# Kernel optimization log

Hardware: AMD Instinct MI355X
Metric: run time of the kernel (lower is better)

## Reference

```python
import jax, jax.numpy as jnp
import numpy as np

T, B, E, H = 2048, 2, 1024, 16
D = E // H  # head_dim = 64

def setup_inputs() -> dict:
    key = jax.random.key(0)
    ks = jax.random.split(key, 9)
    s = 1.0 / np.sqrt(E)
    return {
        "query": jax.random.normal(ks[0], (T, B, E), dtype=jnp.float32),
        "Wq": jax.random.normal(ks[1], (E, E), dtype=jnp.float32) * s,
        "bq": jax.random.normal(ks[2], (E,), dtype=jnp.float32) * 0.02,
        "Wk": jax.random.normal(ks[3], (E, E), dtype=jnp.float32) * s,
        "bk": jax.random.normal(ks[4], (E,), dtype=jnp.float32) * 0.02,
        "Wv": jax.random.normal(ks[5], (E, E), dtype=jnp.float32) * s,
        "bv": jax.random.normal(ks[6], (E,), dtype=jnp.float32) * 0.02,
        "Wo": jax.random.normal(ks[7], (E, E), dtype=jnp.float32) * s,
        "bo": jax.random.normal(ks[8], (E,), dtype=jnp.float32) * 0.02,
    }

def reference(query, Wq, bq, Wk, bk, Wv, bv, Wo, bo):
    # query: [T, B, E] (fairseq Time x Batch x Channel layout)
    t, b, e = query.shape
    scaling = D ** -0.5
    q = (query @ Wq.T + bq) * scaling          # [T,B,E], scaled like fairseq
    k = query @ Wk.T + bk                      # self-attention: k,v from query
    v = query @ Wv.T + bv
    # split heads: [T,B,H,D]
    q = q.reshape(t, b, H, D)
    k = k.reshape(t, b, H, D)
    v = v.reshape(t, b, H, D)
    # attn weights: [B,H,T(tgt),S(src)]
    scores = jnp.einsum("tbhd,sbhd->bhts", q, k)
    probs = jax.nn.softmax(scores, axis=-1)
    # attend: [T,B,H,D] -> [T,B,E]
    ctx = jnp.einsum("bhts,sbhd->tbhd", probs, v).reshape(t, b, e)
    return ctx @ Wo.T + bo                     # [T,B,E]
```

## Files before the change

kernel.cpp:

```cpp
#include <hip/hip_runtime.h>
#include <hip/hip_bf16.h>
#include <math.h>

#define TT 2048
#define BB 2
#define EE 1024
#define HH 16
#define DD 64
#define RR (TT*BB)

typedef __bf16 bf16x8 __attribute__((ext_vector_type(8)));
typedef float  floatx4 __attribute__((ext_vector_type(4)));

__device__ __forceinline__ unsigned short f2b(float f) {
    union { float f; unsigned u; } x{f};
    return (unsigned short)((x.u + 0x7FFFu + ((x.u >> 16) & 1u)) >> 16);
}
__device__ __forceinline__ float b2f_lo(unsigned u) {
    union { unsigned u; float f; } x{u << 16}; return x.f;
}
__device__ __forceinline__ float b2f_hi(unsigned u) {
    union { unsigned u; float f; } x{u & 0xffff0000u}; return x.f;
}

__device__ __forceinline__ float exp2_fast(float x) {
    return __builtin_amdgcn_exp2f(x);
}

typedef const __attribute__((address_space(1))) unsigned int as1_u32;
typedef __attribute__((address_space(3))) unsigned int as3_u32;
__device__ __forceinline__ void gload16(const void* g, void* l) {
    __builtin_amdgcn_global_load_lds((as1_u32*)g, (as3_u32*)l, 16, 0, 0);
}

#define SCALE_Q 0.18033688011112042f

__device__ __forceinline__ int swz(int r) {
    return (r & 7) ^ (((r >> 3) & 3) << 1);
}

__global__ __launch_bounds__(256)
void pack_bf16(const float* __restrict__ x,  const float* __restrict__ wq,
               const float* __restrict__ wk, const float* __restrict__ wv,
               const float* __restrict__ wo, unsigned short* __restrict__ base,
               unsigned short* __restrict__ wob)
{
    const size_t M4 = (size_t)4 << 20, M7 = (size_t)7 << 20;
    const size_t e0 = ((size_t)blockIdx.x * 256 + threadIdx.x) * 8;
    const float* src;
    unsigned short* dst;
    if (e0 < M4) {
        src = x + e0; dst = base + e0;
    } else if (e0 < M7) {
        const int seg = (int)((e0 >> 20) - 4);
        const float* wsrc[3] = {wq, wk, wv};
        src = wsrc[seg] + (e0 & ((1u << 20) - 1));
        dst = base + e0;
    } else {
        src = wo + (e0 - M7); dst = wob + (e0 - M7);
    }
    const float4 a = *(const float4*)src;
    const float4 b = *(const float4*)(src + 4);
    union { unsigned short u[8]; uint4 v; } p;
    p.u[0] = f2b(a.x); p.u[1] = f2b(a.y); p.u[2] = f2b(a.z); p.u[3] = f2b(a.w);
    p.u[4] = f2b(b.x); p.u[5] = f2b(b.y); p.u[6] = f2b(b.z); p.u[7] = f2b(b.w);
    *(uint4*)dst = p.v;
}

template<int MODE>
__global__ __launch_bounds__(256)
void gemm_mfma(const unsigned short* __restrict__ A,
               const unsigned short* __restrict__ Bw,
               const float* __restrict__ b0, const float* __restrict__ b1,
               const float* __restrict__ b2,
               void* __restrict__ out0, void* __restrict__ out1,
               void* __restrict__ out2)
{
    constexpr int BM = 128;
    constexpr int BN = (MODE == 0) ? 128 : 64;
    constexpr int MT = 4;
    constexpr int NT = (MODE == 0) ? 4 : 2;
    constexpr int RA = BM / 32;
    constexpr int RB = BN / 32;
    constexpr int SMEM = (MODE == 0) ? 34816 : 24576;
    __shared__ __align__(16) unsigned char smem[SMEM];
    unsigned short* ldsA = (unsigned short*)smem;
    unsigned short* ldsB = (unsigned short*)(smem + BM * 128);

    const int tid  = threadIdx.x;
    const int w    = tid >> 6;
    const int lane = tid & 63;
    const int quad = lane >> 4;
    const int l15  = lane & 15;
    const int wm   = w & 1;
    const int wn   = w >> 1;
    const int i0   = blockIdx.x * BM;
    const int j0   = blockIdx.y * BN;

    const unsigned short* ga[RA];
    const unsigned short* gb[RB];
    #pragma unroll
    for (int r = 0; r < RA; ++r) {
        const int slot = r * 256 + tid;
        const int row  = slot >> 3;
        const int gc   = (slot & 7) ^ swz(row);
        ga[r] = A + (size_t)(i0 + row) * EE + gc * 8;
    }
    #pragma unroll
    for (int r = 0; r < RB; ++r) {
        const int slot = r * 256 + tid;
        const int row  = slot >> 3;
        const int gc   = (slot & 7) ^ swz(row);
        gb[r] = Bw + (size_t)(j0 + row) * EE + gc * 8;
    }

    int ofsA[2][MT], ofsB[2][NT];
    #pragma unroll
    for (int mt = 0; mt < MT; ++mt) {
        const int row = wm * 64 + mt * 16 + l15;
        #pragma unroll
        for (int ks = 0; ks < 2; ++ks)
            ofsA[ks][mt] = row * 64 + (((ks * 4 + quad) ^ swz(row)) << 3);
    }
    #pragma unroll
    for (int nt = 0; nt < NT; ++nt) {
        const int col = wn * (BN / 2) + nt * 16 + l15;
        #pragma unroll
        for (int ks = 0; ks < 2; ++ks)
            ofsB[ks][nt] = col * 64 + (((ks * 4 + quad) ^ swz(col)) << 3);
    }

    floatx4 acc[MT][NT];
    #pragma unroll
    for (int mt = 0; mt < MT; ++mt)
        #pragma unroll
        for (int nt = 0; nt < NT; ++nt)
            acc[mt][nt] = (floatx4){0.f, 0.f, 0.f, 0.f};

    for (int kk = 0; kk < EE; kk += 64) {
        __syncthreads();
        #pragma unroll
        for (int r = 0; r < RA; ++r)
            gload16(ga[r] + kk, ldsA + (r * 256 + w * 64) * 8);
        #pragma unroll
        for (int r = 0; r < RB; ++r)
            gload16(gb[r] + kk, ldsB + (r * 256 + w * 64) * 8);
        __syncthreads();

        #pragma unroll
        for (int ks = 0; ks < 2; ++ks) {
            bf16x8 af[MT], bfr[NT];
            #pragma unroll
            for (int mt = 0; mt < MT; ++mt)
                af[mt] = __builtin_bit_cast(bf16x8, *(const uint4*)&ldsA[ofsA[ks][mt]]);
            #pragma unroll
            for (int nt = 0; nt < NT; ++nt)
                bfr[nt] = __builtin_bit_cast(bf16x8, *(const uint4*)&ldsB[ofsB[ks][nt]]);
            #pragma unroll
            for (int mt = 0; mt < MT; ++mt)
                #pragma unroll
                for (int nt = 0; nt < NT; ++nt)
                    acc[mt][nt] = __builtin_amdgcn_mfma_f32_16x16x32_bf16(
                        af[mt], bfr[nt], acc[mt][nt], 0, 0, 0);
        }
    }

    if (MODE == 1) {
        float* dst = (float*)out0;
        #pragma unroll
        for (int nt = 0; nt < NT; ++nt) {
            const int j = j0 + wn * 32 + nt * 16 + l15;
            const float bb = b0[j];
            #pragma unroll
            for (int mt = 0; mt < MT; ++mt) {
                const int i = i0 + wm * 64 + mt * 16 + quad * 4;
                #pragma unroll
                for (int r2 = 0; r2 < 4; ++r2)
                    dst[(size_t)(i + r2) * EE + j] = acc[mt][nt][r2] + bb;
            }
        }
    } else {
        const int which = j0 >> 10;
        const float scale = (which == 0) ? SCALE_Q : 1.0f;
        const float* bias = (which == 0) ? b0 : (which == 1) ? b1 : b2;
        if (which < 2) {
            unsigned short* dst = (unsigned short*)(which == 0 ? out0 : out1);
            #pragma unroll
            for (int nt = 0; nt < NT; ++nt) {
                const int j = (j0 & 1023) + wn * 64 + nt * 16 + l15;
                const int h = j >> 6, d = j & 63;
                const float bb = bias[j];
                #pragma unroll
                for (int mt = 0; mt < MT; ++mt) {
                    const int i = i0 + wm * 64 + mt * 16 + quad * 4;
                    #pragma unroll
                    for (int r2 = 0; r2 < 4; ++r2) {
                        const int ii = i + r2;
                        const int t = ii >> 1, b = ii & 1;
                        dst[((size_t)(b * HH + h) * TT + t) * DD + d] =
                            f2b((acc[mt][nt][r2] + bb) * scale);
                    }
                }
            }
        } else {
            __syncthreads();
            unsigned short* tr = (unsigned short*)smem + (size_t)w * 64 * 68;
            #pragma unroll
            for (int nt = 0; nt < NT; ++nt) {
                const int jl = nt * 16 + l15;
                const float bb = bias[(j0 & 1023) + wn * 64 + jl];
                #pragma unroll
                for (int mt = 0; mt < MT; ++mt) {
                    const int il0 = mt * 16 + quad * 4;
                    ushort4 h4;
                    h4.x = f2b(acc[mt][nt][0] + bb);
                    h4.y = f2b(acc[mt][nt][1] + bb);
                    h4.z = f2b(acc[mt][nt][2] + bb);
                    h4.w = f2b(acc[mt][nt][3] + bb);
                    *(ushort4*)&tr[jl * 68 + il0] = h4;
                }
            }
            __syncthreads();
            const int jg = (j0 & 1023) + wn * 64 + lane;
            const int h = jg >> 6, d = jg & 63;
            const int tb = (i0 + wm * 64) >> 1;
            const unsigned short* rp = tr + (size_t)lane * 68;
            unsigned short* dstV = (unsigned short*)out2;
            #pragma unroll
            for (int g = 0; g < 4; ++g) {
                union { unsigned short u[8]; uint4 v; } pe, po;
                #pragma unroll
                for (int k = 0; k < 8; ++k) {
                    pe.u[k] = rp[(g * 8 + k) * 2];
                    po.u[k] = rp[(g * 8 + k) * 2 + 1];
                }
                *(uint4*)&dstV[((size_t)(0 * HH + h) * DD + d) * TT + tb + g * 8] = pe.v;
                *(uint4*)&dstV[((size_t)(1 * HH + h) * DD + d) * TT + tb + g * 8] = po.v;
            }
        }
    }
}

__global__ __launch_bounds__(256)
void attn_mfma(const unsigned short* __restrict__ Q,
               const unsigned short* __restrict__ K,
               const unsigned short* __restrict__ Vt,
               unsigned short* __restrict__ cpart,
               float* __restrict__ lsumbuf)
{
    __shared__ __align__(16) unsigned short ksm[2][64 * 64];
    __shared__ __align__(16) unsigned short vtm[2][64 * 64];

    const int tid  = threadIdx.x;
    const int w    = tid >> 6;
    const int lane = tid & 63;
    const int quad = lane >> 4;
    const int l15  = lane & 15;
    const int bh   = blockIdx.x;
    const int tt   = blockIdx.y;
    const int half = blockIdx.z;

    const unsigned short* Qh = Q  + (size_t)bh * TT * DD;
    const unsigned short* Kh = K  + (size_t)bh * TT * DD;
    const unsigned short* Vh = Vt + (size_t)bh * DD * TT;

    const int q0w  = tt * 128 + w * 32;
    const int key0 = half * 1024;

    bf16x8 qf[2][2];
    #pragma unroll
    for (int qn = 0; qn < 2; ++qn)
        #pragma unroll
        for (int kd = 0; kd < 2; ++kd)
            qf[qn][kd] = __builtin_bit_cast(bf16x8,
                *(const uint4*)&Qh[(size_t)(q0w + qn * 16 + l15) * DD + kd * 32 + quad * 8]);

    const unsigned short* kg[4];
    #pragma unroll
    for (int r = 0; r < 4; ++r) {
        const int slot = r * 256 + tid;
        const int row  = slot >> 3;
        const int gc   = (slot & 7) ^ swz(row);
        kg[r] = Kh + (size_t)(key0 + row) * DD + gc * 8;
    }
    const unsigned short* vg[4];
    #pragma unroll
    for (int r = 0; r < 4; ++r) {
        const int s512 = (r & 1) * 256 + tid;
        const int rowd = s512 >> 3;
        const int gc   = (s512 & 7) ^ swz(rowd);
        vg[r] = Vh + (size_t)rowd * TT + key0 + (r >> 1) * 64 + gc * 8;
    }

    int ofsKA[4][2], ofsVB[4][2];
    #pragma unroll
    for (int mt = 0; mt < 4; ++mt) {
        const int row = ((mt >> 1) << 5) + ((l15 >> 2) << 3) + ((mt & 1) << 2) + (l15 & 3);
        #pragma unroll
        for (int kd = 0; kd < 2; ++kd)
            ofsKA[mt][kd] = row * 64 + (((kd * 4 + quad) ^ swz(row)) << 3);
    }
    #pragma unroll
    for (int dn = 0; dn < 4; ++dn) {
        const int row = dn * 16 + l15;
        #pragma unroll
        for (int ks = 0; ks < 2; ++ks)
            ofsVB[dn][ks] = row * 64 + (((ks * 4 + quad) ^ swz(row)) << 3);
    }

    floatx4 cacc[4][2];
    #pragma unroll
    for (int dn = 0; dn < 4; ++dn)
        #pragma unroll
        for (int qn = 0; qn < 2; ++qn)
            cacc[dn][qn] = (floatx4){0.f, 0.f, 0.f, 0.f};
    float rs[2] = {0.f, 0.f};

    for (int big = 0; big < 8; ++big) {
        const size_t ko = (size_t)big * 128;
        __syncthreads();
        gload16(kg[0] + ko * DD, &ksm[0][(size_t)(0 * 256 + w * 64) * 8]);
        gload16(kg[1] + ko * DD, &ksm[0][(size_t)(1 * 256 + w * 64) * 8]);
        gload16(kg[2] + ko * DD, &ksm[1][(size_t)(0 * 256 + w * 64) * 8]);
        gload16(kg[3] + ko * DD, &ksm[1][(size_t)(1 * 256 + w * 64) * 8]);
        gload16(vg[0] + ko,      &vtm[0][(size_t)(0 * 256 + w * 64) * 8]);
        gload16(vg[1] + ko,      &vtm[0][(size_t)(1 * 256 + w * 64) * 8]);
        gload16(vg[2] + ko,      &vtm[1][(size_t)(0 * 256 + w * 64) * 8]);
        gload16(vg[3] + ko,      &vtm[1][(size_t)(1 * 256 + w * 64) * 8]);
        __syncthreads();

        #pragma unroll
        for (int sub = 0; sub < 2; ++sub) {
            uint2 pk[4][2];
            #pragma unroll
            for (int mt = 0; mt < 4; ++mt) {
                const bf16x8 ka0 = __builtin_bit_cast(bf16x8, *(const uint4*)&ksm[sub][ofsKA[mt][0]]);
                const bf16x8 ka1 = __builtin_bit_cast(bf16x8, *(const uint4*)&ksm[sub][ofsKA[mt][1]]);
                #pragma unroll
                for (int qn = 0; qn < 2; ++qn) {
                    floatx4 s = (floatx4){0.f, 0.f, 0.f, 0.f};
                    s = __builtin_amdgcn_mfma_f32_16x16x32_bf16(ka0, qf[qn][0], s, 0, 0, 0);
                    s = __builtin_amdgcn_mfma_f32_16x16x32_bf16(ka1, qf[qn][1], s, 0, 0, 0);
                    const float p0 = exp2_fast(s[0]);
                    const float p1 = exp2_fast(s[1]);
                    const float p2 = exp2_fast(s[2]);
                    const float p3 = exp2_fast(s[3]);
                    rs[qn] += (p0 + p1) + (p2 + p3);
                    union { __hip_bfloat162 h2[2]; uint2 u; } c;
                    c.h2[0] = __float22bfloat162_rn(make_float2(p0, p1));
                    c.h2[1] = __float22bfloat162_rn(make_float2(p2, p3));
                    pk[mt][qn] = c.u;
                }
            }
            bf16x8 pa[2][2];
            #pragma unroll
            for (int qn = 0; qn < 2; ++qn) {
                union { uint2 d[2]; uint4 v; } a0, a1;
                a0.d[0] = pk[0][qn]; a0.d[1] = pk[1][qn];
                a1.d[0] = pk[2][qn]; a1.d[1] = pk[3][qn];
                pa[qn][0] = __builtin_bit_cast(bf16x8, a0.v);
                pa[qn][1] = __builtin_bit_cast(bf16x8, a1.v);
            }
            #pragma unroll
            for (int dn = 0; dn < 4; ++dn) {
                const bf16x8 vb0 = __builtin_bit_cast(bf16x8, *(const uint4*)&vtm[sub][ofsVB[dn][0]]);
                const bf16x8 vb1 = __builtin_bit_cast(bf16x8, *(const uint4*)&vtm[sub][ofsVB[dn][1]]);
                #pragma unroll
                for (int qn = 0; qn < 2; ++qn) {
                    cacc[dn][qn] = __builtin_amdgcn_mfma_f32_16x16x32_bf16(pa[qn][0], vb0, cacc[dn][qn], 0, 0, 0);
                    cacc[dn][qn] = __builtin_amdgcn_mfma_f32_16x16x32_bf16(pa[qn][1], vb1, cacc[dn][qn], 0, 0, 0);
                }
            }
        }
    }

    const int b = bh / HH, hh = bh % HH;
    float rsw[2];
    #pragma unroll
    for (int qn = 0; qn < 2; ++qn) {
        float t = rs[qn];
        t += __shfl_xor(t, 16);
        t += __shfl_xor(t, 32);
        rsw[qn] = t;
    }
    unsigned short* cp = cpart + (size_t)half * RR * EE;
    #pragma unroll
    for (int qn = 0; qn < 2; ++qn) {
        #pragma unroll
        for (int dn = 0; dn < 4; ++dn) {
            const int e = hh * 64 + dn * 16 + l15;
            #pragma unroll
            for (int j = 0; j < 4; ++j) {
                const int t = q0w + qn * 16 + quad * 4 + j;
                cp[(size_t)(t * BB + b) * EE + e] = f2b(cacc[dn][qn][j]);
            }
        }
    }
    if (quad == 0) {
        lsumbuf[(half * BB * HH + bh) * TT + q0w + 0 * 16 + l15] = rsw[0];
        lsumbuf[(half * BB * HH + bh) * TT + q0w + 1 * 16 + l15] = rsw[1];
    }
}

__global__ __launch_bounds__(256)
void combine(const unsigned short* __restrict__ cpart,
             const float* __restrict__ lsumbuf,
             unsigned short* __restrict__ cb)
{
    const int gid = blockIdx.x * 256 + threadIdx.x;
    const int e0 = (gid & 127) * 8;
    const int r  = gid >> 7;
    const int t = r >> 1, b = r & 1;
    const int h = e0 >> 6;
    const int bh = b * HH + h;
    const float inv = 1.0f /
        (lsumbuf[bh * TT + t] + lsumbuf[(BB * HH + bh) * TT + t]);
    const uint4 c0 = *(const uint4*)&cpart[(size_t)r * EE + e0];
    const uint4 c1 = *(const uint4*)&cpart[(size_t)RR * EE + (size_t)r * EE + e0];
    const unsigned u0[4] = {c0.x, c0.y, c0.z, c0.w};
    const unsigned u1[4] = {c1.x, c1.y, c1.z, c1.w};
    union { unsigned u[4]; uint4 v; } o;
    #pragma unroll
    for (int k = 0; k < 4; ++k) {
        const float lo = (b2f_lo(u0[k]) + b2f_lo(u1[k])) * inv;
        const float hi = (b2f_hi(u0[k]) + b2f_hi(u1[k])) * inv;
        union { __hip_bfloat162 h2; unsigned u; } pk;
        pk.h2 = __float22bfloat162_rn(make_float2(lo, hi));
        o.u[k] = pk.u;
    }
    *(uint4*)&cb[(size_t)r * EE + e0] = o.v;
}

extern "C" void kernel_launch(void* const* d_in, const int* in_sizes, int n_in,
                              void* d_out, int out_size, void* d_ws, size_t ws_size,
                              hipStream_t stream)
{
    const float* x  = (const float*)d_in[0];
    const float* Wq = (const float*)d_in[1];
    const float* bq = (const float*)d_in[2];
    const float* Wk = (const float*)d_in[3];
    const float* bk = (const float*)d_in[4];
    const float* Wv = (const float*)d_in[5];
    const float* bv = (const float*)d_in[6];
    const float* Wo = (const float*)d_in[7];
    const float* bo = (const float*)d_in[8];
    float* out = (float*)d_out;

    const size_t M1 = (size_t)1 << 20;
    unsigned short* base  = (unsigned short*)d_ws;
    unsigned short* xb    = base;
    unsigned short* wqkv  = base + 4 * M1;
    unsigned short* cpart = base;
    unsigned short* qb    = base + 8 * M1;
    unsigned short* kb    = base + 12 * M1;
    unsigned short* vtb   = base + 16 * M1;
    unsigned short* cb    = base + 20 * M1;
    unsigned short* wob   = base + 24 * M1;
    float*          lsum  = (float*)(base + 25 * M1);

    dim3 blk(256);

    pack_bf16<<<dim3(4096), blk, 0, stream>>>(x, Wq, Wk, Wv, Wo, base, wob);

    gemm_mfma<0><<<dim3(RR / 128, 3072 / 128), blk, 0, stream>>>(
        xb, wqkv, bq, bk, bv, qb, kb, vtb);

    attn_mfma<<<dim3(BB * HH, TT / 128, 2), blk, 0, stream>>>(qb, kb, vtb, cpart, lsum);

    combine<<<dim3(RR * EE / 8 / 256), blk, 0, stream>>>(cpart, lsum, cb);

    gemm_mfma<1><<<dim3(RR / 128, EE / 64), blk, 0, stream>>>(
        cb, wob, bo, nullptr, nullptr, out, nullptr, nullptr);
}
```

Baseline: 197.5 us.

## Double-buffer LDS tiles in MFMA GEMM to overlap global loads with compute

Splits the GEMM's shared memory into two buffers and prefetches the next K-tile with gload16 while MFMAs run on the current tile. All LDS fragments for the tile are read into registers first, then the next loads are issued, with a sched_barrier keeping the loads ahead of the MFMAs. This removes one __syncthreads per iteration and hides global-to-LDS latency. In exchange it doubles LDS use, which may lower occupancy, and adds register pressure from holding both ks fragment sets.

```diff
diff --git a/kernel.cpp b/kernel.cpp
--- a/kernel.cpp
+++ b/kernel.cpp
@@ -82,10 +82,9 @@
     constexpr int NT = (MODE == 0) ? 4 : 2;
     constexpr int RA = BM / 32;
     constexpr int RB = BN / 32;
-    constexpr int SMEM = (MODE == 0) ? 34816 : 24576;
-    __shared__ __align__(16) unsigned char smem[SMEM];
-    unsigned short* ldsA = (unsigned short*)smem;
-    unsigned short* ldsB = (unsigned short*)(smem + BM * 128);
+    constexpr int ABYTES = BM * 128;
+    constexpr int BUFB   = (BM + BN) * 128;
+    __shared__ __align__(16) unsigned char smem[2 * BUFB];
 
     const int tid  = threadIdx.x;
     const int w    = tid >> 6;
@@ -137,32 +136,58 @@
         for (int nt = 0; nt < NT; ++nt)
             acc[mt][nt] = (floatx4){0.f, 0.f, 0.f, 0.f};
 
+    {
+        unsigned short* nA = (unsigned short*)(smem);
+        unsigned short* nB = (unsigned short*)(smem + ABYTES);
+        #pragma unroll
+        for (int r = 0; r < RA; ++r)
+            gload16(ga[r], nA + (r * 256 + w * 64) * 8);
+        #pragma unroll
+        for (int r = 0; r < RB; ++r)
+            gload16(gb[r], nB + (r * 256 + w * 64) * 8);
+    }
+
+    int cur = 0;
     for (int kk = 0; kk < EE; kk += 64) {
         __syncthreads();
-        #pragma unroll
-        for (int r = 0; r < RA; ++r)
-            gload16(ga[r] + kk, ldsA + (r * 256 + w * 64) * 8);
-        #pragma unroll
-        for (int r = 0; r < RB; ++r)
-            gload16(gb[r] + kk, ldsB + (r * 256 + w * 64) * 8);
-        __syncthreads();
-
+
+        const unsigned short* lA = (const unsigned short*)(smem + cur * BUFB);
+        const unsigned short* lB = (const unsigned short*)(smem + cur * BUFB + ABYTES);
+
+        bf16x8 af[2][MT], bfr[2][NT];
         #pragma unroll
         for (int ks = 0; ks < 2; ++ks) {
-            bf16x8 af[MT], bfr[NT];
             #pragma unroll
             for (int mt = 0; mt < MT; ++mt)
-                af[mt] = __builtin_bit_cast(bf16x8, *(const uint4*)&ldsA[ofsA[ks][mt]]);
+                af[ks][mt] = __builtin_bit_cast(bf16x8, *(const uint4*)&lA[ofsA[ks][mt]]);
             #pragma unroll
             for (int nt = 0; nt < NT; ++nt)
-                bfr[nt] = __builtin_bit_cast(bf16x8, *(const uint4*)&ldsB[ofsB[ks][nt]]);
+                bfr[ks][nt] = __builtin_bit_cast(bf16x8, *(const uint4*)&lB[ofsB[ks][nt]]);
+        }
+
+        if (kk + 64 < EE) {
+            const int nxt = cur ^ 1;
+            unsigned short* nA = (unsigned short*)(smem + nxt * BUFB);
+            unsigned short* nB = (unsigned short*)(smem + nxt * BUFB + ABYTES);
+            #pragma unroll
+            for (int r = 0; r < RA; ++r)
+                gload16(ga[r] + kk + 64, nA + (r * 256 + w * 64) * 8);
+            #pragma unroll
+            for (int r = 0; r < RB; ++r)
+                gload16(gb[r] + kk + 64, nB + (r * 256 + w * 64) * 8);
+        }
+        __builtin_amdgcn_sched_barrier(0);
+
+        #pragma unroll
+        for (int ks = 0; ks < 2; ++ks)
             #pragma unroll
             for (int mt = 0; mt < MT; ++mt)
                 #pragma unroll
                 for (int nt = 0; nt < NT; ++nt)
                     acc[mt][nt] = __builtin_amdgcn_mfma_f32_16x16x32_bf16(
-                        af[mt], bfr[nt], acc[mt][nt], 0, 0, 0);
-        }
+                        af[ks][mt], bfr[ks][nt], acc[mt][nt], 0, 0, 0);
+
+        cur ^= 1;
     }
 
     if (MODE == 1) {
```

New measurement: 189.5 us. -4.1%, faster.
